# Kernel optimization log

Hardware: AMD Instinct MI355X
Metric: run time of the kernel (lower is better)

Reference implementation:

```python
import jax, jax.numpy as jnp
import numpy as np


def gcn_conv(x, W, b, src, dst, n_nodes):
    # PyG GCNConv: out = D^{-1/2} (A+I) D^{-1/2} X W + b  (self-loops already in src/dst)
    h = x @ W  # [N, F_out]
    ones = jnp.ones(src.shape[0], dtype=h.dtype)
    deg = jax.ops.segment_sum(ones, dst, num_segments=n_nodes)  # in-degree incl. self-loop
    dinv = jnp.where(deg > 0, jax.lax.rsqrt(deg), 0.0)
    norm = dinv[src] * dinv[dst]  # [E]
    msg = h[src] * norm[:, None]  # gather + scale, [E, F_out]
    out = jax.ops.segment_sum(msg, dst, num_segments=n_nodes)  # scatter-add
    return out + b


def setup_inputs() -> dict:
    key = jax.random.key(0)
    ks = jax.random.split(key, 5)
    N, E, F_in, H, F_out = 50000, 800000, 128, 128, 64
    x = jax.random.normal(ks[0], (N, F_in), dtype=jnp.float32)
    edge_index = jax.random.randint(ks[1], (2, E), 0, N, dtype=jnp.int64)
    W1 = jax.random.normal(ks[2], (F_in, H), dtype=jnp.float32) / np.sqrt(F_in)
    b1 = jnp.zeros((H,), dtype=jnp.float32)
    W3 = jax.random.normal(ks[3], (H, F_out), dtype=jnp.float32) / np.sqrt(H)
    b3 = jnp.zeros((F_out,), dtype=jnp.float32)
    W4 = jax.random.normal(ks[4], (H, F_out), dtype=jnp.float32) / np.sqrt(H)
    b4 = jnp.zeros((F_out,), dtype=jnp.float32)
    return {"x": x, "edge_index": edge_index, "W1": W1, "b1": b1,
            "W3": W3, "b3": b3, "W4": W4, "b4": b4}


def reference(x, edge_index, W1, b1, W3, b3, W4, b4):
    n_nodes = x.shape[0]
    loops = jnp.arange(n_nodes, dtype=edge_index.dtype)
    src = jnp.concatenate([edge_index[0], loops])
    dst = jnp.concatenate([edge_index[1], loops])
    h = jax.nn.relu(gcn_conv(x, W1, b1, src, dst, n_nodes))  # dropout p=0.0 is identity
    mean = gcn_conv(h, W3, b3, src, dst, n_nodes)
    std = gcn_conv(h, W4, b4, src, dst, n_nodes)
    return (mean, std)
```

## Files before the change

kernel.cpp:

```cpp
#include <hip/hip_runtime.h>

typedef unsigned int uint_t;
typedef unsigned short ushort_t;

constexpr int MAXDEG = 64;

static __device__ __forceinline__ uint_t f2bf_bits(float f) {
  uint_t u = __builtin_bit_cast(uint_t, f);
  return (u + 0x7fffu + ((u >> 16) & 1u)) >> 16;
}
static __device__ __forceinline__ uint_t pack_bf2(float lo, float hi) {
  return f2bf_bits(lo) | (f2bf_bits(hi) << 16);
}
static __device__ __forceinline__ float bf_lo(uint_t u) {
  return __builtin_bit_cast(float, u << 16);
}
static __device__ __forceinline__ float bf_hi(uint_t u) {
  return __builtin_bit_cast(float, u & 0xffff0000u);
}

typedef __attribute__((ext_vector_type(2))) uint_t v2u;
typedef __attribute__((ext_vector_type(8))) short  short8_t;
typedef __attribute__((ext_vector_type(4))) float  f32x4_t;

static __device__ __forceinline__ void stnt_u2(uint_t* p, uint_t a, uint_t b) {
  v2u t; t.x = a; t.y = b;
  __builtin_nontemporal_store(t, (v2u*)p);
}

static inline size_t align256(size_t x) { return (x + 255) & ~(size_t)255; }

__global__ __launch_bounds__(256) void bucket_scatter_kernel(
    const int* __restrict__ src, const int* __restrict__ dst,
    uint2* __restrict__ buckets, int* __restrict__ bucketcnt,
    int E, int C, int shift, int NB) {
  __shared__ int hist[512];
  __shared__ int base[512];
  const int tid = threadIdx.x;
  const int e0 = blockIdx.x * 2048;

  for (int i = tid; i < NB; i += 256) hist[i] = 0;
  __syncthreads();

  int dd[8], ss[8], slot[8];
#pragma unroll
  for (int i = 0; i < 8; ++i) {
    int e = e0 + tid + i * 256;
    bool ok = (e < E);
    dd[i] = ok ? dst[e] : -1;
    ss[i] = ok ? src[e] : 0;
    slot[i] = ok ? atomicAdd(&hist[dd[i] >> shift], 1) : 0;
  }
  __syncthreads();

  for (int i = tid; i < NB; i += 256) {
    int c = hist[i];
    base[i] = (c > 0) ? atomicAdd(&bucketcnt[i], c) : 0;
  }
  __syncthreads();

#pragma unroll
  for (int i = 0; i < 8; ++i) {
    if (dd[i] < 0) continue;
    int b = dd[i] >> shift;
    int pos = base[b] + slot[i];
    if (pos >= 0 && pos < C)
      buckets[(size_t)b * C + pos] = make_uint2((uint_t)dd[i], (uint_t)ss[i]);
  }
}

template<typename IdxT, int WIN>
__global__ __launch_bounds__(256) void bucket_to_rows_kernel(
    const uint2* __restrict__ buckets, const int* __restrict__ bucketcnt,
    IdxT* __restrict__ edge, int* __restrict__ deg, int Nn, int C, int shift) {
  __shared__ __align__(16) IdxT rows[WIN * MAXDEG];
  __shared__ int cnt[WIN];
  const int tid = threadIdx.x;
  const int b = blockIdx.x;
  const int node0 = b << shift;
  const int RANGE = 1 << shift;
  int ec = bucketcnt[b];
  if (ec > C) ec = C;
  if (ec < 0) ec = 0;
  const uint2* bb = buckets + (size_t)b * C;

  for (int w0 = 0; w0 < RANGE; w0 += WIN) {
    for (int i = tid; i < WIN; i += 256) cnt[i] = 0;
    __syncthreads();
    for (int i = tid; i < ec; i += 256) {
      uint2 it = bb[i];
      int local = (int)it.x - node0 - w0;
      if (local >= 0 && local < WIN) {
        int sl = atomicAdd(&cnt[local], 1);
        if (sl < MAXDEG) rows[local * MAXDEG + sl] = (IdxT)it.y;
      }
    }
    __syncthreads();
    const int nbase = node0 + w0;
    constexpr int PER = (MAXDEG * sizeof(IdxT)) / 16;
    const uint4* rv = (const uint4*)rows;
    uint4* ev = (uint4*)(edge + (size_t)nbase * MAXDEG);
    for (int i = tid; i < WIN * PER; i += 256) {
      int node = nbase + i / PER;
      if (node < Nn) ev[i] = rv[i];
    }
    for (int i = tid; i < WIN; i += 256) {
      int node = nbase + i;
      if (node < Nn) deg[node] = cnt[i];
    }
    __syncthreads();
  }
}

__global__ __launch_bounds__(256) void pack_w_kernel(
    const float* __restrict__ W1, const float* __restrict__ W3,
    const float* __restrict__ W4,
    ushort_t* __restrict__ B1hi, ushort_t* __restrict__ B1lo,
    ushort_t* __restrict__ B2hi, ushort_t* __restrict__ B2lo,
    int* __restrict__ bucketcnt) {
  if (blockIdx.x == 0) {
    bucketcnt[threadIdx.x] = 0;
    bucketcnt[threadIdx.x + 256] = 0;
  }
  const bool w1 = (blockIdx.x < 8);
  int u = (w1 ? blockIdx.x : blockIdx.x - 8) * 256 + threadIdx.x;
  int l = u & 63, kk = (u >> 6) & 3, t = u >> 8;
  int q = l >> 4, c = l & 15;
  int n = t * 16 + c;
  short8_t vh, vl;
#pragma unroll
  for (int j = 0; j < 8; ++j) {
    int k = kk * 32 + q * 8 + j;
    float w;
    if (w1)          w = W1[(size_t)k * 128 + n];
    else if (n < 64) w = W3[(size_t)k * 64 + n];
    else             w = W4[(size_t)k * 64 + (n - 64)];
    uint_t hb = f2bf_bits(w);
    float wl = w - __builtin_bit_cast(float, hb << 16);
    vh[j] = (short)hb;
    vl[j] = (short)f2bf_bits(wl);
  }
  ushort_t* ph = w1 ? B1hi : B2hi;
  ushort_t* pl = w1 ? B1lo : B2lo;
  *(short8_t*)(ph + (size_t)u * 8) = vh;
  *(short8_t*)(pl + (size_t)u * 8) = vl;
}

__global__ __launch_bounds__(256) void gemm1_mfma_kernel(
    const float* __restrict__ X, const ushort_t* __restrict__ Bhi,
    const ushort_t* __restrict__ Blo, ushort_t* __restrict__ outG, int Nrows) {
  const int tid = threadIdx.x;
  const int wid = tid >> 6;
  const int lane = tid & 63;
  const int q = lane >> 4;
  const int c = lane & 15;
  const int rowbase = blockIdx.x * 64 + wid * 16;

  f32x4_t acc[8];
#pragma unroll
  for (int t = 0; t < 8; ++t) acc[t] = (f32x4_t){0.f, 0.f, 0.f, 0.f};

  int arow = rowbase + c;
  int ars = (arow < Nrows) ? arow : (Nrows - 1);
  const float* abase = X + (size_t)ars * 128 + q * 8;

#pragma unroll
  for (int kk = 0; kk < 4; ++kk) {
    float4 xa = *(const float4*)(abase + kk * 32);
    float4 xb = *(const float4*)(abase + kk * 32 + 4);
    float xf[8] = {xa.x, xa.y, xa.z, xa.w, xb.x, xb.y, xb.z, xb.w};
    short8_t ahi, alo;
#pragma unroll
    for (int j = 0; j < 8; ++j) {
      float f = xf[j];
      uint_t hb = f2bf_bits(f);
      ahi[j] = (short)hb;
      float fl = f - __builtin_bit_cast(float, hb << 16);
      alo[j] = (short)f2bf_bits(fl);
    }
#pragma unroll
    for (int t = 0; t < 8; ++t) {
      const size_t fo = ((size_t)(t * 4 + kk) * 64 + lane) * 8;
      short8_t bh = *(const short8_t*)(Bhi + fo);
      short8_t bl = *(const short8_t*)(Blo + fo);
      acc[t] = __builtin_amdgcn_mfma_f32_16x16x32_bf16(ahi, bh, acc[t], 0, 0, 0);
      acc[t] = __builtin_amdgcn_mfma_f32_16x16x32_bf16(ahi, bl, acc[t], 0, 0, 0);
      acc[t] = __builtin_amdgcn_mfma_f32_16x16x32_bf16(alo, bh, acc[t], 0, 0, 0);
    }
  }

#pragma unroll
  for (int t = 0; t < 8; ++t) {
#pragma unroll
    for (int rr = 0; rr < 4; ++rr) {
      int row = rowbase + q * 4 + rr;
      if (row < Nrows)
        outG[(size_t)row * 128 + t * 16 + c] = (ushort_t)f2bf_bits(acc[t][rr]);
    }
  }
}

__global__ __launch_bounds__(256) void gemm2_mfma_kernel(
    const ushort_t* __restrict__ Xbf, const ushort_t* __restrict__ Bhi,
    const ushort_t* __restrict__ Blo, const float* __restrict__ b3,
    const float* __restrict__ b4, float* __restrict__ outM,
    float* __restrict__ outS, int Nrows) {
  const int tid = threadIdx.x;
  const int wid = tid >> 6;
  const int lane = tid & 63;
  const int q = lane >> 4;
  const int c = lane & 15;
  const int rowbase = blockIdx.x * 64 + wid * 16;

  f32x4_t acc[8];
#pragma unroll
  for (int t = 0; t < 8; ++t) acc[t] = (f32x4_t){0.f, 0.f, 0.f, 0.f};

  int arow = rowbase + c;
  int ars = (arow < Nrows) ? arow : (Nrows - 1);
  const ushort_t* abase = Xbf + (size_t)ars * 128 + q * 8;

#pragma unroll
  for (int kk = 0; kk < 4; ++kk) {
    short8_t a = __builtin_nontemporal_load((const short8_t*)(abase + kk * 32));
#pragma unroll
    for (int t = 0; t < 8; ++t) {
      const size_t fo = ((size_t)(t * 4 + kk) * 64 + lane) * 8;
      short8_t bh = *(const short8_t*)(Bhi + fo);
      short8_t bl = *(const short8_t*)(Blo + fo);
      acc[t] = __builtin_amdgcn_mfma_f32_16x16x32_bf16(a, bh, acc[t], 0, 0, 0);
      acc[t] = __builtin_amdgcn_mfma_f32_16x16x32_bf16(a, bl, acc[t], 0, 0, 0);
    }
  }

#pragma unroll
  for (int t = 0; t < 8; ++t) {
    float bias = (t < 4) ? b3[t * 16 + c] : b4[(t - 4) * 16 + c];
    float* obase = (t < 4) ? (outM + t * 16 + c) : (outS + (t - 4) * 16 + c);
#pragma unroll
    for (int rr = 0; rr < 4; ++rr) {
      int row = rowbase + q * 4 + rr;
      if (row < Nrows)
        __builtin_nontemporal_store(acc[t][rr] + bias, obase + (size_t)row * 64);
    }
  }
}

template<int EPI, bool SRCDV, typename IdxT>
__global__ __launch_bounds__(256) void aggregate_kernel(
    const uint_t* __restrict__ g, const int* __restrict__ deg,
    const IdxT* __restrict__ edge, const float* __restrict__ b1,
    uint_t* __restrict__ out, int Nn) {
  const int wave = threadIdx.x >> 6;
  const int lane = threadIdx.x & 63;
  const int n = blockIdx.x * 4 + wave;
  if (n >= Nn) return;
  const int dn = deg[n];
  const int cnt = (dn > 63) ? 63 : dn;
  const float sc = rsqrtf((float)(dn + 1));

  int vl = n;
  if (lane >= 1 && lane <= cnt) vl = (int)edge[(size_t)n * MAXDEG + (lane - 1)];
  float wl = 0.f;
  if (lane == 0)        wl = SRCDV ? sc : 1.f;
  else if (lane <= cnt) wl = SRCDV ? rsqrtf((float)(deg[vl] + 1)) : 1.f;

  const int h = lane >> 5;
  const int c = lane & 31;
  const uint_t* gc = g + c * 2;

  float a0 = 0.f, a1 = 0.f, a2 = 0.f, a3 = 0.f;
  const int entries = cnt + 1;
  const int npairs = (entries + 1) >> 1;

  int p = 0;
  for (; p + 4 <= npairs; p += 4) {
    int ss[4]; float ww[4]; uint2 uu[4];
#pragma unroll
    for (int t = 0; t < 4; ++t) {
      int j = 2 * (p + t) + h;
      ss[t] = __shfl(vl, j);
      ww[t] = __shfl(wl, j);
    }
#pragma unroll
    for (int t = 0; t < 4; ++t)
      uu[t] = *(const uint2*)(gc + (size_t)ss[t] * 64);
#pragma unroll
    for (int t = 0; t < 4; ++t) {
      a0 = fmaf(ww[t], bf_lo(uu[t].x), a0);
      a1 = fmaf(ww[t], bf_hi(uu[t].x), a1);
      a2 = fmaf(ww[t], bf_lo(uu[t].y), a2);
      a3 = fmaf(ww[t], bf_hi(uu[t].y), a3);
    }
  }
  for (; p < npairs; ++p) {
    int j = 2 * p + h;
    int s0 = __shfl(vl, j);
    float w0 = __shfl(wl, j);
    uint2 u = *(const uint2*)(gc + (size_t)s0 * 64);
    a0 = fmaf(w0, bf_lo(u.x), a0);
    a1 = fmaf(w0, bf_hi(u.x), a1);
    a2 = fmaf(w0, bf_lo(u.y), a2);
    a3 = fmaf(w0, bf_hi(u.y), a3);
  }

  a0 += __shfl_xor(a0, 32);
  a1 += __shfl_xor(a1, 32);
  a2 += __shfl_xor(a2, 32);
  a3 += __shfl_xor(a3, 32);

  if (h == 0) {
    if (EPI == 1) {
      float4 b = ((const float4*)b1)[c];
      a0 = fmaxf(fmaf(sc, a0, b.x), 0.f) * sc;
      a1 = fmaxf(fmaf(sc, a1, b.y), 0.f) * sc;
      a2 = fmaxf(fmaf(sc, a2, b.z), 0.f) * sc;
      a3 = fmaxf(fmaf(sc, a3, b.w), 0.f) * sc;
    } else {
      a0 *= sc; a1 *= sc; a2 *= sc; a3 *= sc;
    }
    stnt_u2(out + (size_t)n * 64 + c * 2, pack_bf2(a0, a1), pack_bf2(a2, a3));
  }
}

extern "C" void kernel_launch(void* const* d_in, const int* in_sizes, int n_in,
                              void* d_out, int out_size, void* d_ws, size_t ws_size,
                              hipStream_t stream) {
  const float* x  = (const float*)d_in[0];
  const int*   ei = (const int*)d_in[1];
  const float* W1 = (const float*)d_in[2];
  const float* b1 = (const float*)d_in[3];
  const float* W3 = (const float*)d_in[4];
  const float* b3 = (const float*)d_in[5];
  const float* W4 = (const float*)d_in[6];
  const float* b4 = (const float*)d_in[7];

  const int N = in_sizes[0] / 128;
  const int E = in_sizes[1] / 2;
  const int* src = ei;
  const int* dst = ei + E;
  const bool small = (N <= 65535);
  const size_t esz = small ? sizeof(ushort_t) : sizeof(int);

  int shift = 7;
  while (((N + (1 << shift) - 1) >> shift) > 512) ++shift;
  const int NB = (N + (1 << shift) - 1) >> shift;
  const int C = (E / NB) * 3 / 2 + 512;

  char* w = (char*)d_ws;
  size_t off = 0;
  auto carve = [&](size_t bytes) { void* p = w + off; off = align256(off + bytes); return p; };
  int*      deg       = (int*)carve((size_t)N * sizeof(int));
  int*      bucketcnt = (int*)carve(512 * sizeof(int));
  uint2*    buckets   = (uint2*)carve((size_t)NB * C * sizeof(uint2));
  void*     edge      = carve((size_t)N * MAXDEG * esz);
  uint_t*   bufG      = (uint_t*)carve((size_t)N * 64 * sizeof(uint_t));
  uint_t*   bufH      = (uint_t*)carve((size_t)N * 64 * sizeof(uint_t));
  ushort_t* B1hi      = (ushort_t*)carve((size_t)16384 * sizeof(ushort_t));
  ushort_t* B1lo      = (ushort_t*)carve((size_t)16384 * sizeof(ushort_t));
  ushort_t* B2hi      = (ushort_t*)carve((size_t)16384 * sizeof(ushort_t));
  ushort_t* B2lo      = (ushort_t*)carve((size_t)16384 * sizeof(ushort_t));

  float* out_mean = (float*)d_out;
  float* out_std  = out_mean + (size_t)N * 64;

  const int gblocks = (N + 63) / 64;
  const int ablocks = (N + 3) / 4;
  const int sblocks = (E + 2047) / 2048;

  pack_w_kernel<<<16, 256, 0, stream>>>(W1, W3, W4, B1hi, B1lo, B2hi, B2lo, bucketcnt);
  bucket_scatter_kernel<<<sblocks, 256, 0, stream>>>(src, dst, buckets, bucketcnt, E, C, shift, NB);

  if (small) {
    ushort_t* es = (ushort_t*)edge;
    bucket_to_rows_kernel<ushort_t, 128><<<NB, 256, 0, stream>>>(
        buckets, bucketcnt, es, deg, N, C, shift);
    gemm1_mfma_kernel<<<gblocks, 256, 0, stream>>>(x, B1hi, B1lo, (ushort_t*)bufG, N);
    aggregate_kernel<1, true,  ushort_t><<<ablocks, 256, 0, stream>>>(bufG, deg, es, b1, bufH, N);
    aggregate_kernel<2, false, ushort_t><<<ablocks, 256, 0, stream>>>(bufH, deg, es, nullptr, bufG, N);
  } else {
    int* es = (int*)edge;
    bucket_to_rows_kernel<int, 128><<<NB, 256, 0, stream>>>(
        buckets, bucketcnt, es, deg, N, C, shift);
    gemm1_mfma_kernel<<<gblocks, 256, 0, stream>>>(x, B1hi, B1lo, (ushort_t*)bufG, N);
    aggregate_kernel<1, true,  int><<<ablocks, 256, 0, stream>>>(bufG, deg, es, b1, bufH, N);
    aggregate_kernel<2, false, int><<<ablocks, 256, 0, stream>>>(bufH, deg, es, nullptr, bufG, N);
  }
  gemm2_mfma_kernel<<<gblocks, 256, 0, stream>>>(
      (const ushort_t*)bufG, B2hi, B2lo, b3, b4, out_mean, out_std, N);
}
```

Measured before the change: 126.2 us.

## Fuse second aggregation with second GEMM through shared memory

The second aggregation now writes its normalized bf16 rows into an LDS tile, and the same block runs the MFMA GEMM against the concatenated W3/W4 weights straight from LDS. This drops one kernel launch and the global write and re-read of the intermediate aggregated features. In exchange each wave now aggregates 16 rows one after another instead of one row per wave, so fewer waves are in flight to hide gather latency, and the GEMM phase waits on a block barrier. Edge rows with high degree can also leave the rest of the block idle at that barrier.

```diff
diff --git a/kernel.cpp b/kernel.cpp
--- a/kernel.cpp
+++ b/kernel.cpp
@@ -200,54 +200,8 @@
   }
 }
 
-__global__ __launch_bounds__(256) void gemm2_mfma_kernel(
-    const ushort_t* __restrict__ Xbf, const ushort_t* __restrict__ Bhi,
-    const ushort_t* __restrict__ Blo, const float* __restrict__ b3,
-    const float* __restrict__ b4, float* __restrict__ outM,
-    float* __restrict__ outS, int Nrows) {
-  const int tid = threadIdx.x;
-  const int wid = tid >> 6;
-  const int lane = tid & 63;
-  const int q = lane >> 4;
-  const int c = lane & 15;
-  const int rowbase = blockIdx.x * 64 + wid * 16;
-
-  f32x4_t acc[8];
-#pragma unroll
-  for (int t = 0; t < 8; ++t) acc[t] = (f32x4_t){0.f, 0.f, 0.f, 0.f};
-
-  int arow = rowbase + c;
-  int ars = (arow < Nrows) ? arow : (Nrows - 1);
-  const ushort_t* abase = Xbf + (size_t)ars * 128 + q * 8;
-
-#pragma unroll
-  for (int kk = 0; kk < 4; ++kk) {
-    short8_t a = __builtin_nontemporal_load((const short8_t*)(abase + kk * 32));
-#pragma unroll
-    for (int t = 0; t < 8; ++t) {
-      const size_t fo = ((size_t)(t * 4 + kk) * 64 + lane) * 8;
-      short8_t bh = *(const short8_t*)(Bhi + fo);
-      short8_t bl = *(const short8_t*)(Blo + fo);
-      acc[t] = __builtin_amdgcn_mfma_f32_16x16x32_bf16(a, bh, acc[t], 0, 0, 0);
-      acc[t] = __builtin_amdgcn_mfma_f32_16x16x32_bf16(a, bl, acc[t], 0, 0, 0);
-    }
-  }
-
-#pragma unroll
-  for (int t = 0; t < 8; ++t) {
-    float bias = (t < 4) ? b3[t * 16 + c] : b4[(t - 4) * 16 + c];
-    float* obase = (t < 4) ? (outM + t * 16 + c) : (outS + (t - 4) * 16 + c);
-#pragma unroll
-    for (int rr = 0; rr < 4; ++rr) {
-      int row = rowbase + q * 4 + rr;
-      if (row < Nrows)
-        __builtin_nontemporal_store(acc[t][rr] + bias, obase + (size_t)row * 64);
-    }
-  }
-}
-
-template<int EPI, bool SRCDV, typename IdxT>
-__global__ __launch_bounds__(256) void aggregate_kernel(
+template<typename IdxT>
+__global__ __launch_bounds__(256) void aggregate1_kernel(
     const uint_t* __restrict__ g, const int* __restrict__ deg,
     const IdxT* __restrict__ edge, const float* __restrict__ b1,
     uint_t* __restrict__ out, int Nn) {
@@ -262,8 +216,8 @@
   int vl = n;
   if (lane >= 1 && lane <= cnt) vl = (int)edge[(size_t)n * MAXDEG + (lane - 1)];
   float wl = 0.f;
-  if (lane == 0)        wl = SRCDV ? sc : 1.f;
-  else if (lane <= cnt) wl = SRCDV ? rsqrtf((float)(deg[vl] + 1)) : 1.f;
+  if (lane == 0)        wl = sc;
+  else if (lane <= cnt) wl = rsqrtf((float)(deg[vl] + 1));
 
   const int h = lane >> 5;
   const int c = lane & 31;
@@ -310,16 +264,122 @@
   a3 += __shfl_xor(a3, 32);
 
   if (h == 0) {
-    if (EPI == 1) {
-      float4 b = ((const float4*)b1)[c];
-      a0 = fmaxf(fmaf(sc, a0, b.x), 0.f) * sc;
-      a1 = fmaxf(fmaf(sc, a1, b.y), 0.f) * sc;
-      a2 = fmaxf(fmaf(sc, a2, b.z), 0.f) * sc;
-      a3 = fmaxf(fmaf(sc, a3, b.w), 0.f) * sc;
-    } else {
-      a0 *= sc; a1 *= sc; a2 *= sc; a3 *= sc;
-    }
+    float4 b = ((const float4*)b1)[c];
+    a0 = fmaxf(fmaf(sc, a0, b.x), 0.f) * sc;
+    a1 = fmaxf(fmaf(sc, a1, b.y), 0.f) * sc;
+    a2 = fmaxf(fmaf(sc, a2, b.z), 0.f) * sc;
+    a3 = fmaxf(fmaf(sc, a3, b.w), 0.f) * sc;
     stnt_u2(out + (size_t)n * 64 + c * 2, pack_bf2(a0, a1), pack_bf2(a2, a3));
+  }
+}
+
+template<typename IdxT>
+__global__ __launch_bounds__(256) void agg2_gemm2_kernel(
+    const uint_t* __restrict__ g, const int* __restrict__ deg,
+    const IdxT* __restrict__ edge,
+    const ushort_t* __restrict__ Bhi, const ushort_t* __restrict__ Blo,
+    const float* __restrict__ b3, const float* __restrict__ b4,
+    float* __restrict__ outM, float* __restrict__ outS, int Nn) {
+  __shared__ uint_t lds_h[64][68];
+  const int tid = threadIdx.x;
+  const int wid = tid >> 6;
+  const int lane = tid & 63;
+  const int rowbase = blockIdx.x * 64;
+
+  {
+    const int h = lane >> 5;
+    const int c = lane & 31;
+    const uint_t* gc = g + c * 2;
+    for (int i = 0; i < 16; ++i) {
+      const int r = wid * 16 + i;
+      const int n = rowbase + r;
+      if (n >= Nn) {
+        if (h == 0) { lds_h[r][c * 2] = 0; lds_h[r][c * 2 + 1] = 0; }
+        continue;
+      }
+      const int dn = deg[n];
+      const int cnt = (dn > 63) ? 63 : dn;
+      const float sc = rsqrtf((float)(dn + 1));
+      int vl = n;
+      if (lane >= 1 && lane <= cnt) vl = (int)edge[(size_t)n * MAXDEG + (lane - 1)];
+      const float wl = (lane <= cnt) ? 1.f : 0.f;
+
+      float a0 = 0.f, a1 = 0.f, a2 = 0.f, a3 = 0.f;
+      const int npairs = (cnt + 2) >> 1;
+      int p = 0;
+      for (; p + 4 <= npairs; p += 4) {
+        int ss[4]; float ww[4]; uint2 uu[4];
+#pragma unroll
+        for (int t = 0; t < 4; ++t) {
+          int j = 2 * (p + t) + h;
+          ss[t] = __shfl(vl, j);
+          ww[t] = __shfl(wl, j);
+        }
+#pragma unroll
+        for (int t = 0; t < 4; ++t)
+          uu[t] = *(const uint2*)(gc + (size_t)ss[t] * 64);
+#pragma unroll
+        for (int t = 0; t < 4; ++t) {
+          a0 = fmaf(ww[t], bf_lo(uu[t].x), a0);
+          a1 = fmaf(ww[t], bf_hi(uu[t].x), a1);
+          a2 = fmaf(ww[t], bf_lo(uu[t].y), a2);
+          a3 = fmaf(ww[t], bf_hi(uu[t].y), a3);
+        }
+      }
+      for (; p < npairs; ++p) {
+        int j = 2 * p + h;
+        int s0 = __shfl(vl, j);
+        float w0 = __shfl(wl, j);
+        uint2 u = *(const uint2*)(gc + (size_t)s0 * 64);
+        a0 = fmaf(w0, bf_lo(u.x), a0);
+        a1 = fmaf(w0, bf_hi(u.x), a1);
+        a2 = fmaf(w0, bf_lo(u.y), a2);
+        a3 = fmaf(w0, bf_hi(u.y), a3);
+      }
+      a0 += __shfl_xor(a0, 32);
+      a1 += __shfl_xor(a1, 32);
+      a2 += __shfl_xor(a2, 32);
+      a3 += __shfl_xor(a3, 32);
+      if (h == 0) {
+        a0 *= sc; a1 *= sc; a2 *= sc; a3 *= sc;
+        lds_h[r][c * 2]     = pack_bf2(a0, a1);
+        lds_h[r][c * 2 + 1] = pack_bf2(a2, a3);
+      }
+    }
+  }
+  __syncthreads();
+
+  const int q = lane >> 4;
+  const int c = lane & 15;
+  const int wrowbase = rowbase + wid * 16;
+
+  f32x4_t acc[8];
+#pragma unroll
+  for (int t = 0; t < 8; ++t) acc[t] = (f32x4_t){0.f, 0.f, 0.f, 0.f};
+
+#pragma unroll
+  for (int kk = 0; kk < 4; ++kk) {
+    short8_t a = *(const short8_t*)&lds_h[wid * 16 + c][kk * 16 + q * 4];
+#pragma unroll
+    for (int t = 0; t < 8; ++t) {
+      const size_t fo = ((size_t)(t * 4 + kk) * 64 + lane) * 8;
+      short8_t bh = *(const short8_t*)(Bhi + fo);
+      short8_t bl = *(const short8_t*)(Blo + fo);
+      acc[t] = __builtin_amdgcn_mfma_f32_16x16x32_bf16(a, bh, acc[t], 0, 0, 0);
+      acc[t] = __builtin_amdgcn_mfma_f32_16x16x32_bf16(a, bl, acc[t], 0, 0, 0);
+    }
+  }
+
+#pragma unroll
+  for (int t = 0; t < 8; ++t) {
+    float bias = (t < 4) ? b3[t * 16 + c] : b4[(t - 4) * 16 + c];
+    float* obase = (t < 4) ? (outM + t * 16 + c) : (outS + (t - 4) * 16 + c);
+#pragma unroll
+    for (int rr = 0; rr < 4; ++rr) {
+      int row = wrowbase + q * 4 + rr;
+      if (row < Nn)
+        __builtin_nontemporal_store(acc[t][rr] + bias, obase + (size_t)row * 64);
+    }
   }
 }
 
@@ -376,16 +436,16 @@
     bucket_to_rows_kernel<ushort_t, 128><<<NB, 256, 0, stream>>>(
         buckets, bucketcnt, es, deg, N, C, shift);
     gemm1_mfma_kernel<<<gblocks, 256, 0, stream>>>(x, B1hi, B1lo, (ushort_t*)bufG, N);
-    aggregate_kernel<1, true,  ushort_t><<<ablocks, 256, 0, stream>>>(bufG, deg, es, b1, bufH, N);
-    aggregate_kernel<2, false, ushort_t><<<ablocks, 256, 0, stream>>>(bufH, deg, es, nullptr, bufG, N);
+    aggregate1_kernel<ushort_t><<<ablocks, 256, 0, stream>>>(bufG, deg, es, b1, bufH, N);
+    agg2_gemm2_kernel<ushort_t><<<gblocks, 256, 0, stream>>>(
+        bufH, deg, es, B2hi, B2lo, b3, b4, out_mean, out_std, N);
   } else {
     int* es = (int*)edge;
     bucket_to_rows_kernel<int, 128><<<NB, 256, 0, stream>>>(
         buckets, bucketcnt, es, deg, N, C, shift);
     gemm1_mfma_kernel<<<gblocks, 256, 0, stream>>>(x, B1hi, B1lo, (ushort_t*)bufG, N);
-    aggregate_kernel<1, true,  int><<<ablocks, 256, 0, stream>>>(bufG, deg, es, b1, bufH, N);
-    aggregate_kernel<2, false, int><<<ablocks, 256, 0, stream>>>(bufH, deg, es, nullptr, bufG, N);
-  }
-  gemm2_mfma_kernel<<<gblocks, 256, 0, stream>>>(
-      (const ushort_t*)bufG, B2hi, B2lo, b3, b4, out_mean, out_std, N);
-}
+    aggregate1_kernel<int><<<ablocks, 256, 0, stream>>>(bufG, deg, es, b1, bufH, N);
+    agg2_gemm2_kernel<int><<<gblocks, 256, 0, stream>>>(
+        bufH, deg, es, B2hi, B2lo, b3, b4, out_mean, out_std, N);
+  }
+}
```

Result: slower. 135.4 us (+7.2%).
